# Optimization experiments

Measured on AMD Instinct MI355X. Metric: run time of the kernel, lower is better.

Reference implementation:

```python
import jax, jax.numpy as jnp
import numpy as np

B, D, E, T, P = 65536, 256, 256, 128, 8  # batch, memory_dim, edge_feat_dim, time_dim, num_prototypes
LN_EPS = 1e-6
NORM_EPS = 1e-6


def _layer_norm(x, w, b):
    mu = jnp.mean(x, axis=-1, keepdims=True)
    var = jnp.mean(jnp.square(x - mu), axis=-1, keepdims=True)
    return (x - mu) / jnp.sqrt(var + LN_EPS) * w + b


def setup_inputs() -> dict:
    key = jax.random.key(0)
    ks = jax.random.split(key, 10)
    qin = D + E + T            # query_proj in_features
    gin = 2 * D + T            # gate_proj in_features
    return {
        "raw_memory": jax.random.normal(ks[0], (B, D), dtype=jnp.float32),
        "node_features": jax.random.normal(ks[1], (B, D), dtype=jnp.float32),
        "edge_features": jax.random.normal(ks[2], (B, E), dtype=jnp.float32),
        "time_encoding": jax.random.normal(ks[3], (B, T), dtype=jnp.float32),
        "prototypes": jax.random.normal(ks[4], (B, P, D), dtype=jnp.float32),
        # learned params (xavier gain=0.1 -> small)
        "Wq": jax.random.normal(ks[5], (D, qin), dtype=jnp.float32) * (0.1 * np.sqrt(2.0 / (D + qin))),
        "bq": jnp.zeros((D,), dtype=jnp.float32),
        "Wg": jax.random.normal(ks[6], (1, gin), dtype=jnp.float32) * (0.1 * np.sqrt(2.0 / (1 + gin))),
        "bg": jnp.zeros((1,), dtype=jnp.float32),
        "temperature": jnp.ones((1,), dtype=jnp.float32),
        "ln_w": jnp.ones((D,), dtype=jnp.float32),
        "ln_b": jnp.zeros((D,), dtype=jnp.float32),
    }


def reference(raw_memory, node_features, edge_features, time_encoding, prototypes,
              Wq, bq, Wg, bg, temperature, ln_w, ln_b):
    # query projection (inputs are finite so _sanitize_tensor is identity)
    q_in = jnp.concatenate([raw_memory, edge_features, time_encoding], axis=-1)  # [B, D+E+T]
    query = jnp.tanh(_layer_norm(q_in @ Wq.T + bq, ln_w, ln_b))                   # [B, D]

    # cosine similarity to per-node prototypes (F.normalize uses max(norm, eps))
    qn = query / jnp.maximum(jnp.linalg.norm(query, axis=-1, keepdims=True), NORM_EPS)
    pn = prototypes / jnp.maximum(jnp.linalg.norm(prototypes, axis=-1, keepdims=True), NORM_EPS)
    sim = jnp.clip(jnp.einsum('bd,bpd->bp', qn, pn), -10.0, 10.0)                 # [B, P]
    temp = jnp.clip(temperature, 0.5, 5.0)
    sim = sim / (temp + 0.01)

    attn = jnp.clip(jax.nn.softmax(sim, axis=-1), 0.0, 1.0)                       # [B, P]
    candidate = jnp.clip(jnp.einsum('bp,bpd->bd', attn, prototypes), -5.0, 5.0)   # [B, D]

    # gated update
    g_in = jnp.clip(jnp.concatenate([raw_memory, candidate, time_encoding], axis=-1), -50.0, 50.0)
    gate = jax.nn.sigmoid(jnp.clip(g_in @ Wg.T + bg, -10.0, 10.0))                # [B, 1]
    updated = (1.0 - gate) * raw_memory + gate * candidate
    updated = jnp.clip(_layer_norm(updated, ln_w, ln_b), -10.0, 10.0)
    return updated
```

## Files before the change

kernel.cpp:

```cpp
#include <hip/hip_runtime.h>
#include <cstdint>
#include <cstddef>

#define D 256
#define E 256
#define T 128
#define QIN 640
#define P 8
#define R 16
#define KP 648
#define DP 260

typedef __attribute__((ext_vector_type(8))) short bf16x8;
typedef __attribute__((ext_vector_type(4))) float f32x4;

__device__ __forceinline__ ushort f2bf(float f) {
  uint32_t u = __float_as_uint(f);
  u += 0x7fffu + ((u >> 16) & 1u);
  return (ushort)(u >> 16);
}

__device__ __forceinline__ float rcpf(float x) { return __builtin_amdgcn_rcpf(x); }
__device__ __forceinline__ float rsqf(float x) { return __builtin_amdgcn_rsqf(x); }

__device__ __forceinline__ float fast_tanh(float x) {
  const float e = __expf(2.0f * x);
  return 1.0f - 2.0f * rcpf(e + 1.0f);
}

__device__ __forceinline__ float rsum32(float v) {
#pragma unroll
  for (int o = 16; o > 0; o >>= 1) v += __shfl_xor(v, o, 64);
  return v;
}
__device__ __forceinline__ void rsum32_2(float& a, float& b) {
#pragma unroll
  for (int o = 16; o > 0; o >>= 1) {
    a += __shfl_xor(a, o, 64);
    b += __shfl_xor(b, o, 64);
  }
}

__device__ __forceinline__ float clampf(float x, float lo, float hi) {
  return fminf(fmaxf(x, lo), hi);
}

__global__ void prep_w2_kernel(const float* __restrict__ Wq, ushort* __restrict__ W2) {
  const int idx = blockIdx.x * 256 + threadIdx.x;
  const int n = idx / QIN;
  const int k = idx - n * QIN;
  W2[((((k >> 3) * D + n) << 3)) + (k & 7)] = f2bf(Wq[idx]);
}

__device__ __forceinline__ bf16x8 cvt8(const float* p) {
  const float4 a = *(const float4*)p;
  const float4 b = *(const float4*)(p + 4);
  bf16x8 r;
  r[0] = (short)f2bf(a.x); r[1] = (short)f2bf(a.y);
  r[2] = (short)f2bf(a.z); r[3] = (short)f2bf(a.w);
  r[4] = (short)f2bf(b.x); r[5] = (short)f2bf(b.y);
  r[6] = (short)f2bf(b.z); r[7] = (short)f2bf(b.w);
  return r;
}

template <bool PRE>
__global__ __launch_bounds__(256, 4) void fused_kernel(
    const float* __restrict__ raw, const float* __restrict__ edge,
    const float* __restrict__ tim, const float* __restrict__ proto,
    const float* __restrict__ Wq, const ushort* __restrict__ W2,
    const float* __restrict__ bq, const float* __restrict__ Wg,
    const float* __restrict__ bg, const float* __restrict__ temp,
    const float* __restrict__ lnw, const float* __restrict__ lnb,
    float* __restrict__ out) {
  __shared__ ushort qa[R][KP];
  __shared__ float qpre[R][DP];

  const int tid = threadIdx.x;
  const int r0 = blockIdx.x * R;

#pragma unroll
  for (int it = 0; it < (R * QIN / 4) / 256; ++it) {
    const int flat = it * 256 + tid;
    const int r = flat / (QIN / 4);
    const int p4 = (flat - r * (QIN / 4)) * 4;
    const size_t g = (size_t)(r0 + r);
    float4 v;
    if (p4 < D)          v = *(const float4*)(raw + g * D + p4);
    else if (p4 < D + E) v = *(const float4*)(edge + g * E + (p4 - D));
    else                 v = *(const float4*)(tim + g * T + (p4 - D - E));
    ushort4 h;
    h.x = f2bf(v.x); h.y = f2bf(v.y); h.z = f2bf(v.z); h.w = f2bf(v.w);
    *(ushort4*)&qa[r][p4] = h;
  }
  __syncthreads();

  const int w = tid >> 6;
  const int lane = tid & 63;
  const int lr = lane & 15;
  const int lh = lane >> 4;

  {
    f32x4 acc[4];
#pragma unroll
    for (int c = 0; c < 4; ++c) acc[c] = (f32x4){0.f, 0.f, 0.f, 0.f};

    for (int kb = 0; kb < QIN; kb += 32) {
      const bf16x8 af = *(const bf16x8*)&qa[lr][kb + lh * 8];
#pragma unroll
      for (int c = 0; c < 4; ++c) {
        const int n = w * 64 + c * 16 + lr;
        bf16x8 bv;
        if (PRE) {
          bv = *(const bf16x8*)&W2[(((kb >> 3) + lh) * D + n) << 3];
        } else {
          bv = cvt8(Wq + (size_t)n * QIN + kb + lh * 8);
        }
        acc[c] = __builtin_amdgcn_mfma_f32_16x16x32_bf16(af, bv, acc[c], 0, 0, 0);
      }
    }
#pragma unroll
    for (int c = 0; c < 4; ++c) {
      const int n = w * 64 + c * 16 + lr;
      const float bqv = bq[n];
#pragma unroll
      for (int i = 0; i < 4; ++i) qpre[lh * 4 + i][n] = acc[c][i] + bqv;
    }
  }
  __syncthreads();

  const int h = lane >> 5;
  const int l32 = lane & 31;
  const int d0 = l32 * 4;
  const int d1 = d0 + 128;

  const float4 lw0 = *(const float4*)(lnw + d0);
  const float4 lw1 = *(const float4*)(lnw + d1);
  const float4 lb0 = *(const float4*)(lnb + d0);
  const float4 lb1 = *(const float4*)(lnb + d1);
  const float4 wr0 = *(const float4*)(Wg + d0);
  const float4 wr1 = *(const float4*)(Wg + d1);
  const float4 wc0 = *(const float4*)(Wg + D + d0);
  const float4 wc1 = *(const float4*)(Wg + D + d1);
  const float4 wt4 = *(const float4*)(Wg + 2 * D + d0);
  const float bgv = bg[0];
  const float invt = rcpf(clampf(temp[0], 0.5f, 5.0f) + 0.01f);
  const float lwv[8] = {lw0.x, lw0.y, lw0.z, lw0.w, lw1.x, lw1.y, lw1.z, lw1.w};
  const float lbv[8] = {lb0.x, lb0.y, lb0.z, lb0.w, lb1.x, lb1.y, lb1.z, lb1.w};

#pragma unroll
  for (int j = 0; j < 2; ++j) {
    const int r = j * 8 + w * 2 + h;
    const size_t g = (size_t)(r0 + r);
    const float* pb = proto + g * (size_t)(P * D);

    const float4 ra0 = *(const float4*)(raw + g * D + d0);
    const float4 ra1 = *(const float4*)(raw + g * D + d1);
    const float4 t4  = *(const float4*)(tim + g * T + d0);

    const float4 x0 = *(const float4*)&qpre[r][d0];
    const float4 x1 = *(const float4*)&qpre[r][d1];
    float x[8] = {x0.x, x0.y, x0.z, x0.w, x1.x, x1.y, x1.z, x1.w};
    float s = 0.f, ss = 0.f;
#pragma unroll
    for (int i = 0; i < 8; ++i) { s += x[i]; ss += x[i] * x[i]; }
    rsum32_2(s, ss);
    const float mu = s * (1.0f / 256.0f);
    const float var = ss * (1.0f / 256.0f) - mu * mu;
    const float rstd = rsqf(var + 1e-6f);
    float q[8];
    float qs = 0.f;
#pragma unroll
    for (int i = 0; i < 8; ++i) {
      q[i] = fast_tanh((x[i] - mu) * rstd * lwv[i] + lbv[i]);
      qs += q[i] * q[i];
    }
    const float rq = fminf(rsqf(rsum32(qs)), 1e6f);

    float dt[P], pn[P];
#pragma unroll
    for (int p = 0; p < P; ++p) {
      const float4 p0 = *(const float4*)(pb + (size_t)p * D + d0);
      const float4 p1 = *(const float4*)(pb + (size_t)p * D + d1);
      dt[p] = q[0] * p0.x + q[1] * p0.y + q[2] * p0.z + q[3] * p0.w +
              q[4] * p1.x + q[5] * p1.y + q[6] * p1.z + q[7] * p1.w;
      pn[p] = p0.x * p0.x + p0.y * p0.y + p0.z * p0.z + p0.w * p0.w +
              p1.x * p1.x + p1.y * p1.y + p1.z * p1.z + p1.w * p1.w;
    }
#pragma unroll
    for (int o = 16; o > 0; o >>= 1) {
#pragma unroll
      for (int p = 0; p < P; ++p) {
        dt[p] += __shfl_xor(dt[p], o, 64);
        pn[p] += __shfl_xor(pn[p], o, 64);
      }
    }

    uint64_t pbu = (uint64_t)pb;
    asm volatile("" : "+v"(pbu));
    const float* pb2 = (const float*)pbu;
    float4 C0[P], C1[P];
#pragma unroll
    for (int p = 0; p < P; ++p) {
      C0[p] = *(const float4*)(pb2 + (size_t)p * D + d0);
      C1[p] = *(const float4*)(pb2 + (size_t)p * D + d1);
    }

    float a[P];
#pragma unroll
    for (int p = 0; p < P; ++p) {
      const float rp = fminf(rsqf(pn[p]), 1e6f);
      a[p] = clampf(dt[p] * rq * rp, -10.0f, 10.0f) * invt;
    }
    float m = a[0];
#pragma unroll
    for (int p = 1; p < P; ++p) m = fmaxf(m, a[p]);
    float ssum = 0.f;
#pragma unroll
    for (int p = 0; p < P; ++p) { a[p] = __expf(a[p] - m); ssum += a[p]; }
    const float sinv = rcpf(ssum);
#pragma unroll
    for (int p = 0; p < P; ++p) a[p] = clampf(a[p] * sinv, 0.0f, 1.0f);

    float cd[8] = {0.f, 0.f, 0.f, 0.f, 0.f, 0.f, 0.f, 0.f};
#pragma unroll
    for (int p = 0; p < P; ++p) {
      cd[0] = fmaf(a[p], C0[p].x, cd[0]); cd[1] = fmaf(a[p], C0[p].y, cd[1]);
      cd[2] = fmaf(a[p], C0[p].z, cd[2]); cd[3] = fmaf(a[p], C0[p].w, cd[3]);
      cd[4] = fmaf(a[p], C1[p].x, cd[4]); cd[5] = fmaf(a[p], C1[p].y, cd[5]);
      cd[6] = fmaf(a[p], C1[p].z, cd[6]); cd[7] = fmaf(a[p], C1[p].w, cd[7]);
    }
#pragma unroll
    for (int i = 0; i < 8; ++i) cd[i] = clampf(cd[i], -5.0f, 5.0f);

    const float rr[8] = {ra0.x, ra0.y, ra0.z, ra0.w, ra1.x, ra1.y, ra1.z, ra1.w};
    const float wrv[8] = {wr0.x, wr0.y, wr0.z, wr0.w, wr1.x, wr1.y, wr1.z, wr1.w};
    const float wcv[8] = {wc0.x, wc0.y, wc0.z, wc0.w, wc1.x, wc1.y, wc1.z, wc1.w};
    float gsum = clampf(t4.x, -50.f, 50.f) * wt4.x + clampf(t4.y, -50.f, 50.f) * wt4.y +
                 clampf(t4.z, -50.f, 50.f) * wt4.z + clampf(t4.w, -50.f, 50.f) * wt4.w;
#pragma unroll
    for (int i = 0; i < 8; ++i) {
      gsum += clampf(rr[i], -50.f, 50.f) * wrv[i];
      gsum += clampf(cd[i], -50.f, 50.f) * wcv[i];
    }
    const float z = clampf(rsum32(gsum) + bgv, -10.0f, 10.0f);
    const float gate = rcpf(1.0f + __expf(-z));

    float upd[8];
    float s2 = 0.f, ss2 = 0.f;
#pragma unroll
    for (int i = 0; i < 8; ++i) {
      upd[i] = (1.0f - gate) * rr[i] + gate * cd[i];
      s2 += upd[i]; ss2 += upd[i] * upd[i];
    }
    rsum32_2(s2, ss2);
    const float mu2 = s2 * (1.0f / 256.0f);
    const float var2 = ss2 * (1.0f / 256.0f) - mu2 * mu2;
    const float rstd2 = rsqf(var2 + 1e-6f);
    float4 y0, y1;
    y0.x = clampf((upd[0] - mu2) * rstd2 * lwv[0] + lbv[0], -10.0f, 10.0f);
    y0.y = clampf((upd[1] - mu2) * rstd2 * lwv[1] + lbv[1], -10.0f, 10.0f);
    y0.z = clampf((upd[2] - mu2) * rstd2 * lwv[2] + lbv[2], -10.0f, 10.0f);
    y0.w = clampf((upd[3] - mu2) * rstd2 * lwv[3] + lbv[3], -10.0f, 10.0f);
    y1.x = clampf((upd[4] - mu2) * rstd2 * lwv[4] + lbv[4], -10.0f, 10.0f);
    y1.y = clampf((upd[5] - mu2) * rstd2 * lwv[5] + lbv[5], -10.0f, 10.0f);
    y1.z = clampf((upd[6] - mu2) * rstd2 * lwv[6] + lbv[6], -10.0f, 10.0f);
    y1.w = clampf((upd[7] - mu2) * rstd2 * lwv[7] + lbv[7], -10.0f, 10.0f);
    *(float4*)(out + g * D + d0) = y0;
    *(float4*)(out + g * D + d1) = y1;
  }
}

extern "C" void kernel_launch(void* const* d_in, const int* in_sizes, int n_in,
                              void* d_out, int out_size, void* d_ws, size_t ws_size,
                              hipStream_t stream) {
  const float* raw   = (const float*)d_in[0];
  const float* edge  = (const float*)d_in[2];
  const float* tim   = (const float*)d_in[3];
  const float* proto = (const float*)d_in[4];
  const float* Wq    = (const float*)d_in[5];
  const float* bq    = (const float*)d_in[6];
  const float* Wg    = (const float*)d_in[7];
  const float* bg    = (const float*)d_in[8];
  const float* temp  = (const float*)d_in[9];
  const float* lnw   = (const float*)d_in[10];
  const float* lnb   = (const float*)d_in[11];
  float* out = (float*)d_out;

  const int B = in_sizes[0] / D;
  const int nblk = B / R;

  if (ws_size >= (size_t)QIN * D * sizeof(ushort)) {
    ushort* W2 = (ushort*)d_ws;
    prep_w2_kernel<<<(QIN * D) / 256, 256, 0, stream>>>(Wq, W2);
    fused_kernel<true><<<nblk, 256, 0, stream>>>(raw, edge, tim, proto, Wq, W2,
                                                 bq, Wg, bg, temp, lnw, lnb, out);
  } else {
    fused_kernel<false><<<nblk, 256, 0, stream>>>(raw, edge, tim, proto, Wq,
                                                  (const ushort*)nullptr, bq, Wg,
                                                  bg, temp, lnw, lnb, out);
  }
}
```

Measured before the change: 212.1 us.

## Cut register and LDS pressure to raise occupancy in fused prototype kernel

Aliases the bf16 input staging buffer and the fp32 pre-LN buffer in one shared allocation, adding a barrier after the MFMA loop so the reuse is safe. It raises the launch-bounds occupancy target from 4 to 6 waves. It also moves LN and gate weight loads inside the row loop, disables unrolling of that loop, streams the prototype reloads straight into the FMA accumulation, and drops the softmax max-subtraction. The max-subtraction is safe to drop only because the logits are clamped to a small range. The aim is more resident waves to hide memory latency, at the cost of extra reloads, a barrier, and less instruction-level parallelism.

```diff
diff --git a/kernel.cpp b/kernel.cpp
--- a/kernel.cpp
+++ b/kernel.cpp
@@ -64,7 +64,7 @@
 }
 
 template <bool PRE>
-__global__ __launch_bounds__(256, 4) void fused_kernel(
+__global__ __launch_bounds__(256, 6) void fused_kernel(
     const float* __restrict__ raw, const float* __restrict__ edge,
     const float* __restrict__ tim, const float* __restrict__ proto,
     const float* __restrict__ Wq, const ushort* __restrict__ W2,
@@ -72,8 +72,9 @@
     const float* __restrict__ bg, const float* __restrict__ temp,
     const float* __restrict__ lnw, const float* __restrict__ lnb,
     float* __restrict__ out) {
-  __shared__ ushort qa[R][KP];
-  __shared__ float qpre[R][DP];
+  __shared__ __align__(16) char smem[R * KP * sizeof(ushort)];
+  ushort (*qa)[KP] = (ushort(*)[KP])smem;
+  float (*qpre)[DP] = (float(*)[DP])smem;
 
   const int tid = threadIdx.x;
   const int r0 = blockIdx.x * R;
@@ -118,6 +119,8 @@
         acc[c] = __builtin_amdgcn_mfma_f32_16x16x32_bf16(af, bv, acc[c], 0, 0, 0);
       }
     }
+    __syncthreads();
+
 #pragma unroll
     for (int c = 0; c < 4; ++c) {
       const int n = w * 64 + c * 16 + lr;
@@ -133,21 +136,10 @@
   const int d0 = l32 * 4;
   const int d1 = d0 + 128;
 
-  const float4 lw0 = *(const float4*)(lnw + d0);
-  const float4 lw1 = *(const float4*)(lnw + d1);
-  const float4 lb0 = *(const float4*)(lnb + d0);
-  const float4 lb1 = *(const float4*)(lnb + d1);
-  const float4 wr0 = *(const float4*)(Wg + d0);
-  const float4 wr1 = *(const float4*)(Wg + d1);
-  const float4 wc0 = *(const float4*)(Wg + D + d0);
-  const float4 wc1 = *(const float4*)(Wg + D + d1);
-  const float4 wt4 = *(const float4*)(Wg + 2 * D + d0);
   const float bgv = bg[0];
   const float invt = rcpf(clampf(temp[0], 0.5f, 5.0f) + 0.01f);
-  const float lwv[8] = {lw0.x, lw0.y, lw0.z, lw0.w, lw1.x, lw1.y, lw1.z, lw1.w};
-  const float lbv[8] = {lb0.x, lb0.y, lb0.z, lb0.w, lb1.x, lb1.y, lb1.z, lb1.w};
-
-#pragma unroll
+
+#pragma unroll 1
   for (int j = 0; j < 2; ++j) {
     const int r = j * 8 + w * 2 + h;
     const size_t g = (size_t)(r0 + r);
@@ -167,6 +159,14 @@
     const float mu = s * (1.0f / 256.0f);
     const float var = ss * (1.0f / 256.0f) - mu * mu;
     const float rstd = rsqf(var + 1e-6f);
+
+    const float4 lw0 = *(const float4*)(lnw + d0);
+    const float4 lw1 = *(const float4*)(lnw + d1);
+    const float4 lb0 = *(const float4*)(lnb + d0);
+    const float4 lb1 = *(const float4*)(lnb + d1);
+    const float lwv[8] = {lw0.x, lw0.y, lw0.z, lw0.w, lw1.x, lw1.y, lw1.z, lw1.w};
+    const float lbv[8] = {lb0.x, lb0.y, lb0.z, lb0.w, lb1.x, lb1.y, lb1.z, lb1.w};
+
     float q[8];
     float qs = 0.f;
 #pragma unroll
@@ -195,44 +195,41 @@
       }
     }
 
+    float a[P];
+    float ssum = 0.f;
+#pragma unroll
+    for (int p = 0; p < P; ++p) {
+      const float rp = fminf(rsqf(pn[p]), 1e6f);
+      const float sm = clampf(dt[p] * rq * rp, -10.0f, 10.0f) * invt;
+      a[p] = __expf(sm);
+      ssum += a[p];
+    }
+    const float sinv = rcpf(ssum);
+#pragma unroll
+    for (int p = 0; p < P; ++p) a[p] = clampf(a[p] * sinv, 0.0f, 1.0f);
+
     uint64_t pbu = (uint64_t)pb;
     asm volatile("" : "+v"(pbu));
     const float* pb2 = (const float*)pbu;
-    float4 C0[P], C1[P];
+    float cd[8] = {0.f, 0.f, 0.f, 0.f, 0.f, 0.f, 0.f, 0.f};
 #pragma unroll
     for (int p = 0; p < P; ++p) {
-      C0[p] = *(const float4*)(pb2 + (size_t)p * D + d0);
-      C1[p] = *(const float4*)(pb2 + (size_t)p * D + d1);
-    }
-
-    float a[P];
-#pragma unroll
-    for (int p = 0; p < P; ++p) {
-      const float rp = fminf(rsqf(pn[p]), 1e6f);
-      a[p] = clampf(dt[p] * rq * rp, -10.0f, 10.0f) * invt;
-    }
-    float m = a[0];
-#pragma unroll
-    for (int p = 1; p < P; ++p) m = fmaxf(m, a[p]);
-    float ssum = 0.f;
-#pragma unroll
-    for (int p = 0; p < P; ++p) { a[p] = __expf(a[p] - m); ssum += a[p]; }
-    const float sinv = rcpf(ssum);
-#pragma unroll
-    for (int p = 0; p < P; ++p) a[p] = clampf(a[p] * sinv, 0.0f, 1.0f);
-
-    float cd[8] = {0.f, 0.f, 0.f, 0.f, 0.f, 0.f, 0.f, 0.f};
-#pragma unroll
-    for (int p = 0; p < P; ++p) {
-      cd[0] = fmaf(a[p], C0[p].x, cd[0]); cd[1] = fmaf(a[p], C0[p].y, cd[1]);
-      cd[2] = fmaf(a[p], C0[p].z, cd[2]); cd[3] = fmaf(a[p], C0[p].w, cd[3]);
-      cd[4] = fmaf(a[p], C1[p].x, cd[4]); cd[5] = fmaf(a[p], C1[p].y, cd[5]);
-      cd[6] = fmaf(a[p], C1[p].z, cd[6]); cd[7] = fmaf(a[p], C1[p].w, cd[7]);
+      const float4 c0 = *(const float4*)(pb2 + (size_t)p * D + d0);
+      const float4 c1 = *(const float4*)(pb2 + (size_t)p * D + d1);
+      cd[0] = fmaf(a[p], c0.x, cd[0]); cd[1] = fmaf(a[p], c0.y, cd[1]);
+      cd[2] = fmaf(a[p], c0.z, cd[2]); cd[3] = fmaf(a[p], c0.w, cd[3]);
+      cd[4] = fmaf(a[p], c1.x, cd[4]); cd[5] = fmaf(a[p], c1.y, cd[5]);
+      cd[6] = fmaf(a[p], c1.z, cd[6]); cd[7] = fmaf(a[p], c1.w, cd[7]);
     }
 #pragma unroll
     for (int i = 0; i < 8; ++i) cd[i] = clampf(cd[i], -5.0f, 5.0f);
 
     const float rr[8] = {ra0.x, ra0.y, ra0.z, ra0.w, ra1.x, ra1.y, ra1.z, ra1.w};
+    const float4 wr0 = *(const float4*)(Wg + d0);
+    const float4 wr1 = *(const float4*)(Wg + d1);
+    const float4 wc0 = *(const float4*)(Wg + D + d0);
+    const float4 wc1 = *(const float4*)(Wg + D + d1);
+    const float4 wt4 = *(const float4*)(Wg + 2 * D + d0);
     const float wrv[8] = {wr0.x, wr0.y, wr0.z, wr0.w, wr1.x, wr1.y, wr1.z, wr1.w};
     const float wcv[8] = {wc0.x, wc0.y, wc0.z, wc0.w, wc1.x, wc1.y, wc1.z, wc1.w};
     float gsum = clampf(t4.x, -50.f, 50.f) * wt4.x + clampf(t4.y, -50.f, 50.f) * wt4.y +
```

After: 281.1 us. 32.5% more time.
